# Kernel tuning notes

Hardware: AMD Instinct MI355X
Metric: run time of the kernel (lower is better)

Reference implementation:

```python
import jax, jax.numpy as jnp
import numpy as np
from jax import lax

B, D_MODEL, T = 4, 256, 8192
D_STATE, D_CONV = 16, 4
D_INNER = 2 * D_MODEL          # expand=2.0
DT_RANK = (D_MODEL + 15) // 16 # ceil(d_model/16) = 16
EPS = 1e-5


def setup_inputs() -> dict:
    key = jax.random.key(0)
    ks = jax.random.split(key, 12)
    s = lambda k, shape, scale=0.02: (jax.random.normal(k, shape, jnp.float32) * scale)
    x = jax.random.normal(ks[0], (B, D_MODEL, T), jnp.float32)
    ln_w = jnp.ones((D_MODEL,), jnp.float32)
    ln_b = jnp.zeros((D_MODEL,), jnp.float32)
    in_proj_w = s(ks[1], (2 * D_INNER, D_MODEL))
    conv_w = s(ks[2], (D_INNER, 1, D_CONV), 0.1)
    conv_b = jnp.zeros((D_INNER,), jnp.float32)
    x_proj_w = s(ks[3], (DT_RANK + 2 * D_STATE, D_INNER))
    dt_proj_w = s(ks[4], (D_INNER, DT_RANK), 0.1)
    # bias init so softplus(dt_bias) ~ small positive dt, like mamba_ssm
    dt_proj_b = jnp.log(jnp.expm1(jax.random.uniform(ks[5], (D_INNER,), jnp.float32, 0.001, 0.1)))
    # S4D-real init: A_log = log(1..d_state) broadcast over d_inner
    A_log = jnp.log(jnp.tile(jnp.arange(1, D_STATE + 1, dtype=jnp.float32), (D_INNER, 1)))
    D = jnp.ones((D_INNER,), jnp.float32)
    out_proj_w = s(ks[6], (D_MODEL, D_INNER))
    return {"x": x, "ln_w": ln_w, "ln_b": ln_b, "in_proj_w": in_proj_w,
            "conv_w": conv_w, "conv_b": conv_b, "x_proj_w": x_proj_w,
            "dt_proj_w": dt_proj_w, "dt_proj_b": dt_proj_b, "A_log": A_log,
            "D": D, "out_proj_w": out_proj_w}


def _mamba_block(x, ln_w, ln_b, in_proj_w, conv_w, conv_b, x_proj_w,
                 dt_proj_w, dt_proj_b, A_log, D, out_proj_w):
    # x: (B, C, T)
    residual = x
    xt = jnp.transpose(x, (0, 2, 1))  # (B, T, C)
    # channel layernorm
    mu = jnp.mean(xt, axis=-1, keepdims=True)
    var = jnp.var(xt, axis=-1, keepdims=True)
    xn = (xt - mu) * lax.rsqrt(var + EPS) * ln_w + ln_b
    # in_proj -> x, z
    xz = jnp.einsum('btc,ec->bte', xn, in_proj_w)  # (B,T,2*d_inner)
    x_in, z = jnp.split(xz, 2, axis=-1)
    # causal depthwise conv over time
    xc = jnp.transpose(x_in, (0, 2, 1))  # (B, d_inner, T)
    xc = lax.conv_general_dilated(xc, conv_w, window_strides=(1,),
                                  padding=[(D_CONV - 1, 0)],
                                  dimension_numbers=('NCH', 'OIH', 'NCH'),
                                  feature_group_count=D_INNER)
    xc = xc + conv_b[None, :, None]
    u = jax.nn.silu(jnp.transpose(xc, (0, 2, 1)))  # (B,T,d_inner)
    # x_proj -> dt, B, C
    dbl = jnp.einsum('btd,ed->bte', u, x_proj_w)
    dt, Bm, Cm = jnp.split(dbl, [DT_RANK, DT_RANK + D_STATE], axis=-1)
    delta = jax.nn.softplus(jnp.einsum('btr,dr->btd', dt, dt_proj_w) + dt_proj_b)  # (B,T,d_inner)
    A = -jnp.exp(A_log)  # (d_inner, d_state)
    deltaA = jnp.exp(jnp.einsum('btd,dn->btdn', delta, A))          # (B,T,d,n)
    deltaBu = jnp.einsum('btd,btn->btdn', delta * u, Bm)            # (B,T,d,n)
    # selective scan over time
    def step(h, inp):
        dA_t, dBu_t, C_t = inp
        h = dA_t * h + dBu_t                       # (B,d,n)
        y = jnp.einsum('bdn,bn->bd', h, C_t)
        return h, y
    h0 = jnp.zeros((x.shape[0], D_INNER, D_STATE), x.dtype)
    _, ys = lax.scan(step, h0, (jnp.moveaxis(deltaA, 1, 0),
                                jnp.moveaxis(deltaBu, 1, 0),
                                jnp.moveaxis(Cm, 1, 0)))
    y = jnp.moveaxis(ys, 0, 1) + u * D             # (B,T,d_inner)
    y = y * jax.nn.silu(z)
    out = jnp.einsum('btd,cd->btc', y, out_proj_w)  # (B,T,C)
    return jnp.transpose(out, (0, 2, 1)) + residual


def reference(x, ln_w, ln_b, in_proj_w, conv_w, conv_b, x_proj_w,
              dt_proj_w, dt_proj_b, A_log, D, out_proj_w):
    return _mamba_block(x, ln_w, ln_b, in_proj_w, conv_w, conv_b, x_proj_w,
                        dt_proj_w, dt_proj_b, A_log, D, out_proj_w)
```

## Files before the change

kernel.cpp:

```cpp
#include <hip/hip_runtime.h>

typedef unsigned short u16;
typedef unsigned int u32;
typedef __bf16 bfx8 __attribute__((ext_vector_type(8)));
typedef float f32x4 __attribute__((ext_vector_type(4)));

#define Tn 8192
#define Bn 4
#define MTOT 32768
#define CH 256
#define TC 32

#define OFF_W     0ul
#define OFF_AL2   917504ul
#define OFF_XN    (1ul<<20)
#define OFF_XIN   (17ul<<20)
#define OFF_Z     (49ul<<20)
#define OFF_U     (81ul<<20)
#define OFF_DBLDT (113ul<<20)
#define OFF_BCF   (115ul<<20)
#define OFF_DELTA (119ul<<20)
#define OFF_SD    (151ul<<20)
#define OFF_CC    (153ul<<20)

__device__ __forceinline__ float b2f(u16 h){ return __uint_as_float(((u32)h)<<16); }
__device__ __forceinline__ u16 f2b(float f){
  u32 u = __float_as_uint(f);
  return (u16)((u + 0x7FFFu + ((u>>16)&1u)) >> 16);
}
__device__ __forceinline__ float aexp2(float x){ float r; asm("v_exp_f32 %0, %1" : "=v"(r) : "v"(x)); return r; }
__device__ __forceinline__ float arcp (float x){ float r; asm("v_rcp_f32 %0, %1" : "=v"(r) : "v"(x)); return r; }
__device__ __forceinline__ float alog2(float x){ float r; asm("v_log_f32 %0, %1" : "=v"(r) : "v"(x)); return r; }
__device__ __forceinline__ float fsilu(float a){ return a*arcp(1.f + aexp2(-a*1.44269504f)); }
__device__ __forceinline__ float fsoftplus(float v){
  float r = 0.69314718f*alog2(1.f + aexp2(v*1.44269504f));
  return (v > 20.f) ? v : r;
}
typedef const __attribute__((address_space(1))) void* gp1_t;
typedef __attribute__((address_space(3))) void* lp3_t;
__device__ __forceinline__ void gload_lds16(const void* g, void* l){
  __builtin_amdgcn_global_load_lds((gp1_t)g, (lp3_t)l, 16, 0, 0);
}

__global__ void wconv_k(const float* __restrict__ inw, const float* __restrict__ xpw,
                        const float* __restrict__ dtw, const float* __restrict__ opw,
                        const float* __restrict__ alog, u16* __restrict__ W, float* __restrict__ aL2)
{
  int i = blockIdx.x*256 + threadIdx.x;
  if (i < 262144) { W[i] = f2b(inw[i]); return; }
  if (i < 294912) { int j = i - 262144; int r = j >> 9, k = j & 511;
    float v = (r < 16) ? xpw[r*512 + k] : ((r < 32) ? 0.f : xpw[(r-16)*512 + k]);
    W[i] = f2b(v); return; }
  if (i < 311296) { int j = i - 294912; int d = j >> 5, k = j & 31;
    W[i] = f2b((k < 16) ? dtw[d*16 + k] : 0.f); return; }
  if (i < 442368) { W[i] = f2b(opw[i - 311296]); return; }
  if (i < 450560) { int j = i - 442368; aL2[j] = -__expf(alog[j]) * 1.44269504088896f; return; }
}

__global__ __launch_bounds__(256)
void ln_k(const float* __restrict__ x, const float* __restrict__ lnw,
          const float* __restrict__ lnb, u16* __restrict__ xn)
{
  const int t0 = blockIdx.x*64, b = blockIdx.y;
  const int tid = threadIdx.x, cg = tid>>6, tl = tid&63;
  __shared__ float ps[4][64], pq[4][64], mu[64], rs[64];
  float s = 0.f, q = 0.f;
  for (int ci = 0; ci < 64; ci++){
    int c = ci*4 + cg;
    float v = x[((size_t)(b*256 + c))*Tn + t0 + tl];
    s += v; q += v*v;
  }
  ps[cg][tl] = s; pq[cg][tl] = q;
  __syncthreads();
  if (tid < 64){
    float S = ps[0][tid]+ps[1][tid]+ps[2][tid]+ps[3][tid];
    float Q = pq[0][tid]+pq[1][tid]+pq[2][tid]+pq[3][tid];
    float m = S*(1.f/256.f);
    float var = Q*(1.f/256.f) - m*m;
    mu[tid] = m; rs[tid] = rsqrtf(var + 1e-5f);
  }
  __syncthreads();
  const float w = lnw[tid&255], bb = lnb[tid&255];
  for (int t = 0; t < 64; t++){
    float v = x[((size_t)(b*256 + tid))*Tn + t0 + t];
    xn[((size_t)(b*Tn) + t0 + t)*256 + tid] = f2b((v - mu[t])*rs[t]*w + bb);
  }
}

template<int BN, int EPI>
__global__ __launch_bounds__(256)
void gemm_k(const u16* __restrict__ A, int lda,
            const u16* __restrict__ Bw, int ldb,
            u16* __restrict__ O, u16* __restrict__ O2, float* __restrict__ Of, int ldo,
            const float* __restrict__ bias, int K)
{
  constexpr int NFR = BN/32;
  __shared__ __align__(16) u16 sA[128*32];
  __shared__ __align__(16) u16 sB[BN*32];
  const int tid = threadIdx.x;
  const int m0 = blockIdx.x*128, n0 = blockIdx.y*BN;
  const int lane = tid & 63, wid = tid >> 6;
  const int wr = wid >> 1, wc = wid & 1;
  const int lr = lane & 15, g = lane >> 4;
  const f32x4 fz = {0.f,0.f,0.f,0.f};
  f32x4 acc[4][NFR];
  #pragma unroll
  for (int m=0;m<4;m++)
    #pragma unroll
    for (int n=0;n<NFR;n++) acc[m][n] = fz;
  const int nk = K >> 5;
  for (int kt = 0; kt < nk; ++kt){
    __syncthreads();
    #pragma unroll
    for (int i=0;i<2;i++){ int ci = i*256 + tid;
      gload_lds16(A + (size_t)(m0+(ci>>2))*lda + kt*32 + (ci&3)*8, sA + ci*8); }
    #pragma unroll
    for (int i=0;i<BN/64;i++){ int ci = i*256 + tid;
      gload_lds16(Bw + (size_t)(n0+(ci>>2))*ldb + kt*32 + (ci&3)*8, sB + ci*8); }
    __syncthreads();
    bfx8 af[4], bf[NFR];
    #pragma unroll
    for (int m=0;m<4;m++) af[m] = *(const bfx8*)(sA + (wr*64 + m*16 + lr)*32 + g*8);
    #pragma unroll
    for (int n=0;n<NFR;n++) bf[n] = *(const bfx8*)(sB + (wc*(BN/2) + n*16 + lr)*32 + g*8);
    #pragma unroll
    for (int m=0;m<4;m++)
      #pragma unroll
      for (int n=0;n<NFR;n++)
        acc[m][n] = __builtin_amdgcn_mfma_f32_16x16x32_bf16(af[m], bf[n], acc[m][n], 0, 0, 0);
  }
  #pragma unroll
  for (int m=0;m<4;m++)
    #pragma unroll
    for (int n=0;n<NFR;n++)
      #pragma unroll
      for (int r=0;r<4;r++){
        int row = m0 + wr*64 + m*16 + g*4 + r;
        int col = n0 + wc*(BN/2) + n*16 + lr;
        float v = acc[m][n][r];
        if (EPI == 1){
          O[(size_t)row*ldo + col] = f2b(fsoftplus(v + bias[col]));
        } else if (EPI == 2){
          if (col < 512) O[(size_t)row*512 + col] = f2b(v);
          else           O2[(size_t)row*512 + (col-512)] = f2b(v);
        } else {
          if (col < 32) O[(size_t)row*32 + col] = f2b(v);
          else          Of[(size_t)row*32 + (col-32)] = v;
        }
      }
}

__global__ __launch_bounds__(256)
void gemmot_k(const u16* __restrict__ A, const u16* __restrict__ Bw,
              const float* __restrict__ x, float* __restrict__ out)
{
  __shared__ __align__(16) u16 sA[128*32];
  __shared__ __align__(16) u16 sB[128*32];
  __shared__ float st[64][129];
  const int tid = threadIdx.x;
  const int m0 = blockIdx.x*128, n0 = blockIdx.y*128;
  const int lane = tid & 63, wid = tid >> 6;
  const int wr = wid >> 1, wc = wid & 1;
  const int lr = lane & 15, g = lane >> 4;
  const f32x4 fz = {0.f,0.f,0.f,0.f};
  f32x4 acc[4][4];
  #pragma unroll
  for (int m=0;m<4;m++)
    #pragma unroll
    for (int n=0;n<4;n++) acc[m][n] = fz;
  for (int kt = 0; kt < 16; ++kt){
    __syncthreads();
    #pragma unroll
    for (int i=0;i<2;i++){ int ci = i*256 + tid;
      gload_lds16(A + (size_t)(m0+(ci>>2))*512 + kt*32 + (ci&3)*8, sA + ci*8); }
    #pragma unroll
    for (int i=0;i<2;i++){ int ci = i*256 + tid;
      gload_lds16(Bw + (size_t)(n0+(ci>>2))*512 + kt*32 + (ci&3)*8, sB + ci*8); }
    __syncthreads();
    bfx8 af[4], bf[4];
    #pragma unroll
    for (int m=0;m<4;m++) af[m] = *(const bfx8*)(sA + (wr*64 + m*16 + lr)*32 + g*8);
    #pragma unroll
    for (int n=0;n<4;n++) bf[n] = *(const bfx8*)(sB + (wc*64 + n*16 + lr)*32 + g*8);
    #pragma unroll
    for (int m=0;m<4;m++)
      #pragma unroll
      for (int n=0;n<4;n++)
        acc[m][n] = __builtin_amdgcn_mfma_f32_16x16x32_bf16(af[m], bf[n], acc[m][n], 0, 0, 0);
  }
  const int b = m0 >> 13, t0 = m0 & 8191;
  const int tl = tid & 63, cgrp = tid >> 6;
  for (int hf=0; hf<2; hf++){
    __syncthreads();
    if (wr == hf){
      #pragma unroll
      for (int m=0;m<4;m++)
        #pragma unroll
        for (int n=0;n<4;n++)
          #pragma unroll
          for (int r=0;r<4;r++)
            st[m*16 + g*4 + r][wc*64 + n*16 + lr] = acc[m][n][r];
    }
    __syncthreads();
    const int tg = t0 + hf*64 + tl;
    #pragma unroll
    for (int ci=0; ci<32; ci++){
      int c = cgrp*32 + ci;
      size_t oa = ((size_t)(b*256) + n0 + c)*Tn + tg;
      out[oa] = st[tl][c] + x[oa];
    }
  }
}

__global__ __launch_bounds__(256)
void conv_k(const u16* __restrict__ xin, const float* __restrict__ cw,
            const float* __restrict__ cb, u16* __restrict__ u)
{
  const int t0 = blockIdx.x*32, d0 = blockIdx.y*64, b = blockIdx.z;
  const int tid = threadIdx.x;
  __shared__ float sx[35][64];
  __shared__ float sw[4][64];
  { int d = tid>>2, j = tid&3; sw[j][d] = cw[(d0+d)*4 + j]; }
  for (int i=0;i<9;i++){ int f = i*256 + tid; if (f < 35*64){
      int r = f>>6, dd = f&63; int t = t0 - 3 + r;
      sx[r][dd] = (t >= 0) ? b2f(xin[((size_t)(b*Tn)+t)*512 + d0+dd]) : 0.f; } }
  __syncthreads();
  const float cbv = cb[d0 + (tid&63)];
  for (int oi=0; oi<8; oi++){
    int f = oi*256 + tid; int tr = f>>6, dd = f&63;
    float a = cbv;
    #pragma unroll
    for (int j=0;j<4;j++) a += sw[j][dd]*sx[tr+j][dd];
    u[((size_t)(b*Tn)+t0+tr)*512 + d0+dd] = f2b(fsilu(a));
  }
}

__device__ __forceinline__ void powtree(float r1, float* e){
  float r2 = r1*r1;
  float r3 = r2*r1, r4 = r2*r2;
  float r5 = r4*r1, r6 = r4*r2, r7 = r4*r3, r8 = r4*r4;
  e[0]=r1; e[1]=r2; e[2]=r3; e[3]=r4; e[4]=r5; e[5]=r6; e[6]=r7; e[7]=r8;
  #pragma unroll
  for (int k=0;k<8;k++) e[8+k] = r8*e[k];
}

__global__ __launch_bounds__(256)
void scanA_k(const u16* __restrict__ delta, const u16* __restrict__ u,
             const float* __restrict__ bcf, const float* __restrict__ aL2,
             float* __restrict__ SD, float* __restrict__ CC)
{
  const int ch = blockIdx.x, d = blockIdx.y*256 + threadIdx.x, b = blockIdx.z;
  const int t0 = ch*TC;
  float aL[16], h[16];
  #pragma unroll
  for (int i=0;i<4;i++) *(f32x4*)(aL+4*i) = *(const f32x4*)(aL2 + (size_t)d*16 + 4*i);
  #pragma unroll
  for (int n=0;n<16;n++) h[n] = 0.f;
  bool st = true;
  #pragma unroll
  for (int n=1;n<16;n++) st = st && (fabsf(aL[n] - (n+1)*aL[0]) <= 2e-4f*fabsf(aL[n]));
  const u16* dp = delta + (size_t)(b*Tn + t0)*512 + d;
  const u16* up = u     + (size_t)(b*Tn + t0)*512 + d;
  const float* bp = bcf + (size_t)(b*Tn + t0)*32;
  float sdlt = 0.f;
  const float aL0 = aL[0];
  if (st){
    #pragma unroll 4
    for (int t=0;t<TC;t++){
      float dlt = b2f(dp[(size_t)t*512]);
      float uu  = b2f(up[(size_t)t*512]);
      float Bv[16];
      #pragma unroll
      for (int i=0;i<4;i++) *(f32x4*)(Bv+4*i) = *(const f32x4*)(bp + (size_t)t*32 + 4*i);
      float du = dlt*uu; sdlt += dlt;
      float e[16];
      powtree(aexp2(dlt*aL0), e);
      #pragma unroll
      for (int n=0;n<16;n++)
        h[n] = fmaf(e[n], h[n], du*Bv[n]);
    }
  } else {
    #pragma unroll 2
    for (int t=0;t<TC;t++){
      float dlt = b2f(dp[(size_t)t*512]);
      float uu  = b2f(up[(size_t)t*512]);
      float Bv[16];
      #pragma unroll
      for (int i=0;i<4;i++) *(f32x4*)(Bv+4*i) = *(const f32x4*)(bp + (size_t)t*32 + 4*i);
      float du = dlt*uu; sdlt += dlt;
      #pragma unroll
      for (int n=0;n<16;n++)
        h[n] = fmaf(aexp2(dlt*aL[n]), h[n], du*Bv[n]);
    }
  }
  SD[(size_t)(b*CH+ch)*512 + d] = sdlt;
  size_t o = ((size_t)((b*CH+ch)*512 + d))<<4;
  #pragma unroll
  for (int i=0;i<4;i++)
    *(f32x4*)(CC+o+4*i) = *(f32x4*)(h +4*i);
}

__global__ __launch_bounds__(256)
void scanB_k(const float* __restrict__ SD, const float* __restrict__ aL2, float* __restrict__ CC)
{
  const int gid = blockIdx.x*256 + threadIdx.x;
  const int b = gid >> 13, r = gid & 8191;
  const float aL = aL2[r];
  const float* sdp = SD + (size_t)b*CH*512 + (r>>4);
  const size_t base = (size_t)b*CH*8192 + r;
  float h = 0.f;
  for (int ch=0; ch<CH; ch++){
    float Pv = aexp2(sdp[(size_t)ch*512] * aL);
    size_t idx = base + (size_t)ch*8192;
    float cv = CC[idx];
    CC[idx] = h;
    h = fmaf(Pv, h, cv);
  }
}

__global__ __launch_bounds__(256)
void scanC_k(const u16* __restrict__ delta, const u16* __restrict__ u,
             const float* __restrict__ bcf, const u16* __restrict__ z,
             const float* __restrict__ aL2, const float* __restrict__ h0,
             const float* __restrict__ Dp, u16* __restrict__ yg)
{
  const int ch = blockIdx.x, d = blockIdx.y*256 + threadIdx.x, b = blockIdx.z;
  const int t0 = ch*TC;
  float aL[16], h[16];
  #pragma unroll
  for (int i=0;i<4;i++) *(f32x4*)(aL+4*i) = *(const f32x4*)(aL2 + (size_t)d*16 + 4*i);
  size_t o = ((size_t)((b*CH+ch)*512 + d))<<4;
  #pragma unroll
  for (int i=0;i<4;i++) *(f32x4*)(h+4*i) = *(const f32x4*)(h0+o+4*i);
  bool st = true;
  #pragma unroll
  for (int n=1;n<16;n++) st = st && (fabsf(aL[n] - (n+1)*aL[0]) <= 2e-4f*fabsf(aL[n]));
  const float Dd = Dp[d];
  const float aL0 = aL[0];
  const u16* dp = delta + (size_t)(b*Tn + t0)*512 + d;
  const u16* up = u     + (size_t)(b*Tn + t0)*512 + d;
  const u16* zp = z     + (size_t)(b*Tn + t0)*512 + d;
  const float* bp = bcf + (size_t)(b*Tn + t0)*32;
  u16* yp = yg + (size_t)(b*Tn + t0)*512 + d;
  if (st){
    #pragma unroll 2
    for (int t=0;t<TC;t++){
      float dlt = b2f(dp[(size_t)t*512]);
      float uu  = b2f(up[(size_t)t*512]);
      float zz  = b2f(zp[(size_t)t*512]);
      float Bv[16], Cv[16];
      #pragma unroll
      for (int i=0;i<4;i++){
        *(f32x4*)(Bv+4*i) = *(const f32x4*)(bp + (size_t)t*32 + 4*i);
        *(f32x4*)(Cv+4*i) = *(const f32x4*)(bp + (size_t)t*32 + 16 + 4*i);
      }
      float du = dlt*uu;
      float e[16];
      powtree(aexp2(dlt*aL0), e);
      float p0=0.f, p1=0.f, p2=0.f, p3=0.f;
      #pragma unroll
      for (int n=0;n<16;n+=4){
        h[n]   = fmaf(e[n],   h[n],   du*Bv[n]);   p0 = fmaf(h[n],   Cv[n],   p0);
        h[n+1] = fmaf(e[n+1], h[n+1], du*Bv[n+1]); p1 = fmaf(h[n+1], Cv[n+1], p1);
        h[n+2] = fmaf(e[n+2], h[n+2], du*Bv[n+2]); p2 = fmaf(h[n+2], Cv[n+2], p2);
        h[n+3] = fmaf(e[n+3], h[n+3], du*Bv[n+3]); p3 = fmaf(h[n+3], Cv[n+3], p3);
      }
      float p = (p0+p1) + (p2+p3);
      float gy = (p + uu*Dd) * fsilu(zz);
      yp[(size_t)t*512] = f2b(gy);
    }
  } else {
    #pragma unroll 2
    for (int t=0;t<TC;t++){
      float dlt = b2f(dp[(size_t)t*512]);
      float uu  = b2f(up[(size_t)t*512]);
      float zz  = b2f(zp[(size_t)t*512]);
      float Bv[16], Cv[16];
      #pragma unroll
      for (int i=0;i<4;i++){
        *(f32x4*)(Bv+4*i) = *(const f32x4*)(bp + (size_t)t*32 + 4*i);
        *(f32x4*)(Cv+4*i) = *(const f32x4*)(bp + (size_t)t*32 + 16 + 4*i);
      }
      float du = dlt*uu;
      float p0 = 0.f;
      #pragma unroll
      for (int n=0;n<16;n++){
        h[n] = fmaf(aexp2(dlt*aL[n]), h[n], du*Bv[n]);
        p0 = fmaf(h[n], Cv[n], p0);
      }
      float gy = (p0 + uu*Dd) * fsilu(zz);
      yp[(size_t)t*512] = f2b(gy);
    }
  }
}

extern "C" void kernel_launch(void* const* d_in, const int* in_sizes, int n_in,
                              void* d_out, int out_size, void* d_ws, size_t ws_size,
                              hipStream_t stream)
{
  const float* x    = (const float*)d_in[0];
  const float* lnw  = (const float*)d_in[1];
  const float* lnb  = (const float*)d_in[2];
  const float* inw  = (const float*)d_in[3];
  const float* cw   = (const float*)d_in[4];
  const float* cb   = (const float*)d_in[5];
  const float* xpw  = (const float*)d_in[6];
  const float* dtw  = (const float*)d_in[7];
  const float* dtb  = (const float*)d_in[8];
  const float* alog = (const float*)d_in[9];
  const float* Dp   = (const float*)d_in[10];
  const float* opw  = (const float*)d_in[11];
  float* out = (float*)d_out;
  char* ws = (char*)d_ws;

  u16*   W     = (u16*)(ws + OFF_W);
  float* aL2   = (float*)(ws + OFF_AL2);
  u16*   xn    = (u16*)(ws + OFF_XN);
  u16*   xin   = (u16*)(ws + OFF_XIN);
  u16*   z     = (u16*)(ws + OFF_Z);
  u16*   u     = (u16*)(ws + OFF_U);
  u16*   dblDT = (u16*)(ws + OFF_DBLDT);
  float* bcf   = (float*)(ws + OFF_BCF);
  u16*   delta = (u16*)(ws + OFF_DELTA);
  float* SD    = (float*)(ws + OFF_SD);
  float* CC    = (float*)(ws + OFF_CC);
  u16*   yg    = xin;

  wconv_k<<<1760, 256, 0, stream>>>(inw, xpw, dtw, opw, alog, W, aL2);
  ln_k<<<dim3(Tn/64, Bn), 256, 0, stream>>>(x, lnw, lnb, xn);
  gemm_k<128,2><<<dim3(MTOT/128, 8), 256, 0, stream>>>(xn, 256, W, 256, xin, z, nullptr, 512, nullptr, 256);
  conv_k<<<dim3(Tn/32, 8, Bn), 256, 0, stream>>>(xin, cw, cb, u);
  gemm_k<64,3><<<dim3(MTOT/128, 1), 256, 0, stream>>>(u, 512, W + 262144, 512, dblDT, nullptr, bcf, 0, nullptr, 512);
  gemm_k<128,1><<<dim3(MTOT/128, 4), 256, 0, stream>>>(dblDT, 32, W + 294912, 32, delta, nullptr, nullptr, 512, dtb, 32);
  scanA_k<<<dim3(CH, 2, Bn), 256, 0, stream>>>(delta, u, bcf, aL2, SD, CC);
  scanB_k<<<128, 256, 0, stream>>>(SD, aL2, CC);
  scanC_k<<<dim3(CH, 2, Bn), 256, 0, stream>>>(delta, u, bcf, z, aL2, CC, Dp, yg);
  gemmot_k<<<dim3(MTOT/128, 2), 256, 0, stream>>>(yg, W + 311296, x, out);
}
```

Before: 223.2 us.

## Double-buffer GEMM LDS tiles, cache LN input in LDS, respread scanB blocks

The in-projection and output GEMMs now use two LDS buffers, so the next K-tile's global-to-LDS load is issued while MFMAs run on the current tile, with one barrier per iteration instead of two. The output GEMM epilogue stages results through a smaller 64-column LDS tile in four passes to make room for the extra buffers. That pass adds extra barriers, and a leftover loop writes scratch data to the tile and then breaks out. LayerNorm keeps the loaded x tile in LDS as bf16 instead of reading x from global memory a second time, which adds a small rounding step before normalisation. The inter-chunk scan uses 512 blocks of 64 threads with an unrolled loop, to spread its serial work across more compute units.

```diff
diff --git a/kernel.cpp b/kernel.cpp
--- a/kernel.cpp
+++ b/kernel.cpp
@@ -63,12 +63,14 @@
 {
   const int t0 = blockIdx.x*64, b = blockIdx.y;
   const int tid = threadIdx.x, cg = tid>>6, tl = tid&63;
+  __shared__ u16 sx[256][66];
   __shared__ float ps[4][64], pq[4][64], mu[64], rs[64];
   float s = 0.f, q = 0.f;
   for (int ci = 0; ci < 64; ci++){
     int c = ci*4 + cg;
     float v = x[((size_t)(b*256 + c))*Tn + t0 + tl];
     s += v; q += v*v;
+    sx[c][tl] = f2b(v);
   }
   ps[cg][tl] = s; pq[cg][tl] = q;
   __syncthreads();
@@ -80,9 +82,9 @@
     mu[tid] = m; rs[tid] = rsqrtf(var + 1e-5f);
   }
   __syncthreads();
-  const float w = lnw[tid&255], bb = lnb[tid&255];
+  const float w = lnw[tid], bb = lnb[tid];
   for (int t = 0; t < 64; t++){
-    float v = x[((size_t)(b*256 + tid))*Tn + t0 + t];
+    float v = b2f(sx[tid][t]);
     xn[((size_t)(b*Tn) + t0 + t)*256 + tid] = f2b((v - mu[t])*rs[t]*w + bb);
   }
 }
@@ -95,8 +97,8 @@
             const float* __restrict__ bias, int K)
 {
   constexpr int NFR = BN/32;
-  __shared__ __align__(16) u16 sA[128*32];
-  __shared__ __align__(16) u16 sB[BN*32];
+  __shared__ __align__(16) u16 sA2[2][128*32];
+  __shared__ __align__(16) u16 sB2[2][BN*32];
   const int tid = threadIdx.x;
   const int m0 = blockIdx.x*128, n0 = blockIdx.y*BN;
   const int lane = tid & 63, wid = tid >> 6;
@@ -109,25 +111,33 @@
     #pragma unroll
     for (int n=0;n<NFR;n++) acc[m][n] = fz;
   const int nk = K >> 5;
+
+  auto STAGE = [&](int bi, int kt){
+    #pragma unroll
+    for (int i=0;i<2;i++){ int ci = i*256 + tid;
+      gload_lds16(A + (size_t)(m0+(ci>>2))*lda + kt*32 + (ci&3)*8, &sA2[bi][ci*8]); }
+    #pragma unroll
+    for (int i=0;i<BN/64;i++){ int ci = i*256 + tid;
+      gload_lds16(Bw + (size_t)(n0+(ci>>2))*ldb + kt*32 + (ci&3)*8, &sB2[bi][ci*8]); }
+  };
+
+  STAGE(0, 0);
+  __syncthreads();
   for (int kt = 0; kt < nk; ++kt){
-    __syncthreads();
-    #pragma unroll
-    for (int i=0;i<2;i++){ int ci = i*256 + tid;
-      gload_lds16(A + (size_t)(m0+(ci>>2))*lda + kt*32 + (ci&3)*8, sA + ci*8); }
-    #pragma unroll
-    for (int i=0;i<BN/64;i++){ int ci = i*256 + tid;
-      gload_lds16(Bw + (size_t)(n0+(ci>>2))*ldb + kt*32 + (ci&3)*8, sB + ci*8); }
-    __syncthreads();
+    const int cur = kt & 1;
+    if (kt+1 < nk) STAGE(cur^1, kt+1);
+    const u16* sa = &sA2[cur][0]; const u16* sb = &sB2[cur][0];
     bfx8 af[4], bf[NFR];
     #pragma unroll
-    for (int m=0;m<4;m++) af[m] = *(const bfx8*)(sA + (wr*64 + m*16 + lr)*32 + g*8);
-    #pragma unroll
-    for (int n=0;n<NFR;n++) bf[n] = *(const bfx8*)(sB + (wc*(BN/2) + n*16 + lr)*32 + g*8);
+    for (int m=0;m<4;m++) af[m] = *(const bfx8*)(sa + (wr*64 + m*16 + lr)*32 + g*8);
+    #pragma unroll
+    for (int n=0;n<NFR;n++) bf[n] = *(const bfx8*)(sb + (wc*(BN/2) + n*16 + lr)*32 + g*8);
     #pragma unroll
     for (int m=0;m<4;m++)
       #pragma unroll
       for (int n=0;n<NFR;n++)
         acc[m][n] = __builtin_amdgcn_mfma_f32_16x16x32_bf16(af[m], bf[n], acc[m][n], 0, 0, 0);
+    __syncthreads();
   }
   #pragma unroll
   for (int m=0;m<4;m++)
@@ -154,9 +164,9 @@
 void gemmot_k(const u16* __restrict__ A, const u16* __restrict__ Bw,
               const float* __restrict__ x, float* __restrict__ out)
 {
-  __shared__ __align__(16) u16 sA[128*32];
-  __shared__ __align__(16) u16 sB[128*32];
-  __shared__ float st[64][129];
+  __shared__ __align__(16) u16 sA2[2][128*32];
+  __shared__ __align__(16) u16 sB2[2][128*32];
+  __shared__ float st[64][65];
   const int tid = threadIdx.x;
   const int m0 = blockIdx.x*128, n0 = blockIdx.y*128;
   const int lane = tid & 63, wid = tid >> 6;
@@ -168,25 +178,33 @@
   for (int m=0;m<4;m++)
     #pragma unroll
     for (int n=0;n<4;n++) acc[m][n] = fz;
+
+  auto STAGE = [&](int bi, int kt){
+    #pragma unroll
+    for (int i=0;i<2;i++){ int ci = i*256 + tid;
+      gload_lds16(A + (size_t)(m0+(ci>>2))*512 + kt*32 + (ci&3)*8, &sA2[bi][ci*8]); }
+    #pragma unroll
+    for (int i=0;i<2;i++){ int ci = i*256 + tid;
+      gload_lds16(Bw + (size_t)(n0+(ci>>2))*512 + kt*32 + (ci&3)*8, &sB2[bi][ci*8]); }
+  };
+
+  STAGE(0, 0);
+  __syncthreads();
   for (int kt = 0; kt < 16; ++kt){
-    __syncthreads();
-    #pragma unroll
-    for (int i=0;i<2;i++){ int ci = i*256 + tid;
-      gload_lds16(A + (size_t)(m0+(ci>>2))*512 + kt*32 + (ci&3)*8, sA + ci*8); }
-    #pragma unroll
-    for (int i=0;i<2;i++){ int ci = i*256 + tid;
-      gload_lds16(Bw + (size_t)(n0+(ci>>2))*512 + kt*32 + (ci&3)*8, sB + ci*8); }
-    __syncthreads();
+    const int cur = kt & 1;
+    if (kt+1 < 16) STAGE(cur^1, kt+1);
+    const u16* sa = &sA2[cur][0]; const u16* sb = &sB2[cur][0];
     bfx8 af[4], bf[4];
     #pragma unroll
-    for (int m=0;m<4;m++) af[m] = *(const bfx8*)(sA + (wr*64 + m*16 + lr)*32 + g*8);
-    #pragma unroll
-    for (int n=0;n<4;n++) bf[n] = *(const bfx8*)(sB + (wc*64 + n*16 + lr)*32 + g*8);
+    for (int m=0;m<4;m++) af[m] = *(const bfx8*)(sa + (wr*64 + m*16 + lr)*32 + g*8);
+    #pragma unroll
+    for (int n=0;n<4;n++) bf[n] = *(const bfx8*)(sb + (wc*64 + n*16 + lr)*32 + g*8);
     #pragma unroll
     for (int m=0;m<4;m++)
       #pragma unroll
       for (int n=0;n<4;n++)
         acc[m][n] = __builtin_amdgcn_mfma_f32_16x16x32_bf16(af[m], bf[n], acc[m][n], 0, 0, 0);
+    __syncthreads();
   }
   const int b = m0 >> 13, t0 = m0 & 8191;
   const int tl = tid & 63, cgrp = tid >> 6;
@@ -199,15 +217,36 @@
         for (int n=0;n<4;n++)
           #pragma unroll
           for (int r=0;r<4;r++)
-            st[m*16 + g*4 + r][wc*64 + n*16 + lr] = acc[m][n][r];
+            st[m*16 + g*4 + r][(wc*64 + n*16 + lr)&63 | ((wc*64 + n*16 + lr)>>6)] = acc[m][n][r];
     }
     __syncthreads();
     const int tg = t0 + hf*64 + tl;
     #pragma unroll
-    for (int ci=0; ci<32; ci++){
-      int c = cgrp*32 + ci;
-      size_t oa = ((size_t)(b*256) + n0 + c)*Tn + tg;
-      out[oa] = st[tl][c] + x[oa];
+    for (int ci=0; ci<16; ci++){
+      int c = cgrp*16 + ci + ((wc*0)&0);
+    }
+    break;
+  }
+  for (int hf=0; hf<2; hf++){
+    for (int cp=0; cp<2; cp++){
+      __syncthreads();
+      if (wr == hf && wc == cp){
+        #pragma unroll
+        for (int m=0;m<4;m++)
+          #pragma unroll
+          for (int n=0;n<4;n++)
+            #pragma unroll
+            for (int r=0;r<4;r++)
+              st[m*16 + g*4 + r][n*16 + lr] = acc[m][n][r];
+      }
+      __syncthreads();
+      const int tg = t0 + hf*64 + tl;
+      #pragma unroll
+      for (int ci=0; ci<16; ci++){
+        int c = cgrp*16 + ci;
+        size_t oa = ((size_t)(b*256) + n0 + cp*64 + c)*Tn + tg;
+        out[oa] = st[tl][c] + x[oa];
+      }
     }
   }
 }
@@ -300,15 +339,16 @@
     *(f32x4*)(CC+o+4*i) = *(f32x4*)(h +4*i);
 }
 
-__global__ __launch_bounds__(256)
+__global__ __launch_bounds__(64)
 void scanB_k(const float* __restrict__ SD, const float* __restrict__ aL2, float* __restrict__ CC)
 {
-  const int gid = blockIdx.x*256 + threadIdx.x;
+  const int gid = blockIdx.x*64 + threadIdx.x;
   const int b = gid >> 13, r = gid & 8191;
   const float aL = aL2[r];
   const float* sdp = SD + (size_t)b*CH*512 + (r>>4);
   const size_t base = (size_t)b*CH*8192 + r;
   float h = 0.f;
+  #pragma unroll 4
   for (int ch=0; ch<CH; ch++){
     float Pv = aexp2(sdp[(size_t)ch*512] * aL);
     size_t idx = base + (size_t)ch*8192;
@@ -433,7 +473,7 @@
   gemm_k<64,3><<<dim3(MTOT/128, 1), 256, 0, stream>>>(u, 512, W + 262144, 512, dblDT, nullptr, bcf, 0, nullptr, 512);
   gemm_k<128,1><<<dim3(MTOT/128, 4), 256, 0, stream>>>(dblDT, 32, W + 294912, 32, delta, nullptr, nullptr, 512, dtb, 32);
   scanA_k<<<dim3(CH, 2, Bn), 256, 0, stream>>>(delta, u, bcf, aL2, SD, CC);
-  scanB_k<<<128, 256, 0, stream>>>(SD, aL2, CC);
+  scanB_k<<<512, 64, 0, stream>>>(SD, aL2, CC);
   scanC_k<<<dim3(CH, 2, Bn), 256, 0, stream>>>(delta, u, bcf, z, aL2, CC, Dp, yg);
   gemmot_k<<<dim3(MTOT/128, 2), 256, 0, stream>>>(yg, W + 311296, x, out);
 }
```

New measurement: 235.3 us. +5.4%, slower.
